# Performance work log

Hardware: AMD Instinct MI355X
Metric: run time of the kernel (lower is better)

## Reference

```python
import jax, jax.numpy as jnp
import numpy as np

N = 100000   # nodes
E = 1600000  # edges (avg degree 16)
D_IN, D_HID, D_OUT = 128, 128, 64
BN_EPS = 1e-5


def setup_inputs() -> dict:
    key = jax.random.key(0)
    ks = jax.random.split(key, 12)
    nf_mat = jax.random.normal(ks[0], (N, D_IN), dtype=jnp.float32)
    edge_index = jax.random.randint(ks[1], (2, E), 0, N, dtype=jnp.int32)
    # pre-normalized adjacency weights (GCNConv normalize=True is folded into conv_mat here)
    edge_weight = jax.random.uniform(ks[2], (E,), dtype=jnp.float32) * (1.0 / 16.0)
    def glorot(k, fan_in, fan_out):
        s = jnp.sqrt(6.0 / (fan_in + fan_out)).astype(jnp.float32)
        return jax.random.uniform(k, (fan_in, fan_out), dtype=jnp.float32, minval=-s, maxval=s)
    return {
        "nf_mat": nf_mat,
        "edge_index": edge_index,
        "edge_weight": edge_weight,
        "W0": glorot(ks[3], D_IN, D_HID), "b0": jnp.zeros((D_HID,), jnp.float32),
        "W1": glorot(ks[4], D_HID, D_HID), "b1": jnp.zeros((D_HID,), jnp.float32),
        "W2": glorot(ks[5], D_HID, D_OUT), "b2": jnp.zeros((D_OUT,), jnp.float32),
        "gamma0": jnp.ones((D_HID,), jnp.float32), "beta0": jnp.zeros((D_HID,), jnp.float32),
        "gamma1": jnp.ones((D_HID,), jnp.float32), "beta1": jnp.zeros((D_HID,), jnp.float32),
    }


def _gcn_conv(x, W, b, src, dst, w):
    # GCNConv: aggregate A_norm @ (x W) + b over the sparse edge list
    h = x @ W                                   # [N, F_out]
    msg = h[src] * w[:, None]                   # [E, F_out] gather + scale
    agg = jax.ops.segment_sum(msg, dst, num_segments=N)  # scatter-add -> [N, F_out]
    return agg + b


def _batchnorm(x, gamma, beta):
    # BatchNorm1d over node dimension (training-mode batch statistics, biased var)
    mu = jnp.mean(x, axis=0)
    var = jnp.mean(jnp.square(x - mu), axis=0)
    return gamma * (x - mu) * jax.lax.rsqrt(var + BN_EPS) + beta


def reference(nf_mat, edge_index, edge_weight, W0, b0, W1, b1, W2, b2,
              gamma0, beta0, gamma1, beta1):
    src, dst = edge_index[0], edge_index[1]
    x = nf_mat
    # layer 0: conv -> BN -> ReLU (dropout is identity in eval)
    x = _gcn_conv(x, W0, b0, src, dst, edge_weight)
    x = jax.nn.relu(_batchnorm(x, gamma0, beta0))
    # layer 1
    x = _gcn_conv(x, W1, b1, src, dst, edge_weight)
    x = jax.nn.relu(_batchnorm(x, gamma1, beta1))
    # final conv, then cross-node sum
    x = _gcn_conv(x, W2, b2, src, dst, edge_weight)
    return jnp.sum(x, axis=0)  # [D_OUT]
```

## Files before the change

### kernel.cpp

```cpp
#include <hip/hip_runtime.h>

#define BN_EPS 1e-5f

#define NPB 512
#define NPB_SHIFT 9
#define PB 512
#define WCB 200
#define WCCAP 16
#define CAP 10240
#define NSLICE 16

typedef __attribute__((ext_vector_type(8))) short short8;
typedef __attribute__((ext_vector_type(4))) float floatx4;
typedef __attribute__((ext_vector_type(2))) float floatx2;

__device__ __forceinline__ unsigned short f2bf(float f) {
    unsigned u = __float_as_uint(f);
    unsigned r = u + 0x7FFFu + ((u >> 16) & 1u);
    return (unsigned short)(r >> 16);
}
__device__ __forceinline__ float blo(unsigned v) { return __uint_as_float(v << 16); }
__device__ __forceinline__ float bhi(unsigned v) { return __uint_as_float(v & 0xffff0000u); }

__device__ __forceinline__ uint2 pk8_fp8(const float4 v0, const float4 v1) {
    int lo = 0, hi = 0;
    lo = __builtin_amdgcn_cvt_pk_fp8_f32(v0.x, v0.y, lo, false);
    lo = __builtin_amdgcn_cvt_pk_fp8_f32(v0.z, v0.w, lo, true);
    hi = __builtin_amdgcn_cvt_pk_fp8_f32(v1.x, v1.y, hi, false);
    hi = __builtin_amdgcn_cvt_pk_fp8_f32(v1.z, v1.w, hi, true);
    return make_uint2((unsigned)lo, (unsigned)hi);
}

__global__ __launch_bounds__(256) void wconv(
    const float* __restrict__ W0, const float* __restrict__ W1,
    unsigned short* __restrict__ wt0, unsigned short* __restrict__ wt1,
    float* __restrict__ stats)
{
    const int idx = blockIdx.x * 256 + threadIdx.x;
    const int n = idx >> 7, k = idx & 127;
    wt0[idx] = f2bf(W0[k * 128 + n]);
    wt1[idx] = f2bf(W1[k * 128 + n]);
    if (blockIdx.x < 11) {
        const int o = (blockIdx.x * 256 + threadIdx.x) * 4;
        *(float4*)&stats[o] = make_float4(0.f, 0.f, 0.f, 0.f);
    }
}

__global__ __launch_bounds__(256) void gemm0(
    const float* __restrict__ A, const unsigned short* __restrict__ Wt,
    uint2* __restrict__ C, int M)
{
    __shared__ char lds[53248];
    unsigned short* Al = (unsigned short*)lds;
    unsigned short* Wl = (unsigned short*)(lds + 17408);
    float* Cl = (float*)lds;

    const int tid = threadIdx.x;
    const int r0 = blockIdx.x * 64;

#pragma unroll
    for (int i = 0; i < 16; ++i) {
        const int idx = i * 256 + tid;
        const int n = idx >> 5, q = idx & 31;
        const ushort4 v = ((const ushort4*)Wt)[idx];
        *(ushort4*)&Wl[n * 136 + q * 4] = v;
    }
#pragma unroll
    for (int i = 0; i < 8; ++i) {
        const int row = i * 8 + (tid >> 5), q = tid & 31;
        const int gr = r0 + row;
        float4 v = (gr < M) ? ((const float4*)A)[(size_t)gr * 32 + q]
                            : make_float4(0.f, 0.f, 0.f, 0.f);
        ushort4 o;
        o.x = f2bf(v.x); o.y = f2bf(v.y); o.z = f2bf(v.z); o.w = f2bf(v.w);
        *(ushort4*)&Al[row * 136 + q * 4] = o;
    }
    __syncthreads();

    const int wave = tid >> 6, lane = tid & 63;
    const int lrow = lane & 15, quad = lane >> 4;
    const int n0 = wave * 32;

    floatx4 acc[4][2];
#pragma unroll
    for (int mt = 0; mt < 4; ++mt)
#pragma unroll
        for (int t = 0; t < 2; ++t)
#pragma unroll
            for (int j = 0; j < 4; ++j) acc[mt][t][j] = 0.f;

#pragma unroll
    for (int c = 0; c < 4; ++c) {
        const int k0 = c * 32;
        const short8 b0 = *(const short8*)&Wl[(n0 + lrow) * 136 + k0 + quad * 8];
        const short8 b1 = *(const short8*)&Wl[(n0 + 16 + lrow) * 136 + k0 + quad * 8];
#pragma unroll
        for (int mt = 0; mt < 4; ++mt) {
            const short8 a = *(const short8*)&Al[(mt * 16 + lrow) * 136 + k0 + quad * 8];
            acc[mt][0] = __builtin_amdgcn_mfma_f32_16x16x32_bf16(a, b0, acc[mt][0], 0, 0, 0);
            acc[mt][1] = __builtin_amdgcn_mfma_f32_16x16x32_bf16(a, b1, acc[mt][1], 0, 0, 0);
        }
    }
    __syncthreads();

#pragma unroll
    for (int mt = 0; mt < 4; ++mt)
#pragma unroll
        for (int t = 0; t < 2; ++t)
#pragma unroll
            for (int j = 0; j < 4; ++j)
                Cl[(mt * 16 + quad * 4 + j) * 132 + n0 + t * 16 + lrow] = acc[mt][t][j];
    __syncthreads();

#pragma unroll
    for (int i = 0; i < 4; ++i) {
        const int row = i * 16 + (tid >> 4);
        const int c0 = (tid & 15) * 8;
        const int gr = r0 + row;
        if (gr < M) {
            const float4 v0 = *(float4*)&Cl[row * 132 + c0];
            const float4 v1 = *(float4*)&Cl[row * 132 + c0 + 4];
            C[(size_t)gr * 16 + (c0 >> 3)] = pk8_fp8(v0, v1);
        }
    }
}

__global__ __launch_bounds__(256) void gemm1(
    const unsigned* __restrict__ Ab, const unsigned short* __restrict__ Wt,
    uint2* __restrict__ C,
    const float* __restrict__ sum, const float* __restrict__ sq,
    const float* __restrict__ g, const float* __restrict__ be,
    int M, int N)
{
    __shared__ char lds[53248];
    unsigned short* Al = (unsigned short*)lds;
    unsigned short* Wl = (unsigned short*)(lds + 17408);
    float* AscL = (float*)(lds + 52224);
    float* AshL = AscL + 128;
    float* Cl = (float*)lds;

    const int tid = threadIdx.x;
    const int r0 = blockIdx.x * 64;

    if (tid < 128) {
        float s = 0.f, q = 0.f;
#pragma unroll
        for (int k = 0; k < NSLICE; ++k) {
            s += sum[k * 128 + tid];
            q += sq[k * 128 + tid];
        }
        const float invN = 1.0f / (float)N;
        const float m = s * invN;
        const float var = q * invN - m * m;
        const float rs = rsqrtf(var + BN_EPS);
        AscL[tid] = g[tid] * rs;
        AshL[tid] = be[tid] - g[tid] * m * rs;
    }
    __syncthreads();

#pragma unroll
    for (int i = 0; i < 16; ++i) {
        const int idx = i * 256 + tid;
        const int n = idx >> 5, q = idx & 31;
        const ushort4 v = ((const ushort4*)Wt)[idx];
        *(ushort4*)&Wl[n * 136 + q * 4] = v;
    }
#pragma unroll
    for (int i = 0; i < 4; ++i) {
        const int idx = i * 256 + tid;
        const int row = idx >> 4, qc = idx & 15;
        const int gr = r0 + row;
        uint4 v = (gr < M) ? ((const uint4*)Ab)[(size_t)gr * 16 + qc]
                           : make_uint4(0, 0, 0, 0);
        const float4 a0 = *(const float4*)&AscL[qc * 8];
        const float4 a1 = *(const float4*)&AscL[qc * 8 + 4];
        const float4 b0 = *(const float4*)&AshL[qc * 8];
        const float4 b1 = *(const float4*)&AshL[qc * 8 + 4];
        float x0 = fmaxf(fmaf(a0.x, blo(v.x), b0.x), 0.f);
        float x1 = fmaxf(fmaf(a0.y, bhi(v.x), b0.y), 0.f);
        float x2 = fmaxf(fmaf(a0.z, blo(v.y), b0.z), 0.f);
        float x3 = fmaxf(fmaf(a0.w, bhi(v.y), b0.w), 0.f);
        float x4 = fmaxf(fmaf(a1.x, blo(v.z), b1.x), 0.f);
        float x5 = fmaxf(fmaf(a1.y, bhi(v.z), b1.y), 0.f);
        float x6 = fmaxf(fmaf(a1.z, blo(v.w), b1.z), 0.f);
        float x7 = fmaxf(fmaf(a1.w, bhi(v.w), b1.w), 0.f);
        uint4 o;
        o.x = (unsigned)f2bf(x0) | ((unsigned)f2bf(x1) << 16);
        o.y = (unsigned)f2bf(x2) | ((unsigned)f2bf(x3) << 16);
        o.z = (unsigned)f2bf(x4) | ((unsigned)f2bf(x5) << 16);
        o.w = (unsigned)f2bf(x6) | ((unsigned)f2bf(x7) << 16);
        *(uint4*)&Al[row * 136 + qc * 8] = o;
    }
    __syncthreads();

    const int wave = tid >> 6, lane = tid & 63;
    const int lrow = lane & 15, quad = lane >> 4;
    const int n0 = wave * 32;

    floatx4 acc[4][2];
#pragma unroll
    for (int mt = 0; mt < 4; ++mt)
#pragma unroll
        for (int t = 0; t < 2; ++t)
#pragma unroll
            for (int j = 0; j < 4; ++j) acc[mt][t][j] = 0.f;

#pragma unroll
    for (int c = 0; c < 4; ++c) {
        const int k0 = c * 32;
        const short8 b0 = *(const short8*)&Wl[(n0 + lrow) * 136 + k0 + quad * 8];
        const short8 b1 = *(const short8*)&Wl[(n0 + 16 + lrow) * 136 + k0 + quad * 8];
#pragma unroll
        for (int mt = 0; mt < 4; ++mt) {
            const short8 a = *(const short8*)&Al[(mt * 16 + lrow) * 136 + k0 + quad * 8];
            acc[mt][0] = __builtin_amdgcn_mfma_f32_16x16x32_bf16(a, b0, acc[mt][0], 0, 0, 0);
            acc[mt][1] = __builtin_amdgcn_mfma_f32_16x16x32_bf16(a, b1, acc[mt][1], 0, 0, 0);
        }
    }
    __syncthreads();

#pragma unroll
    for (int mt = 0; mt < 4; ++mt)
#pragma unroll
        for (int t = 0; t < 2; ++t)
#pragma unroll
            for (int j = 0; j < 4; ++j)
                Cl[(mt * 16 + quad * 4 + j) * 132 + n0 + t * 16 + lrow] = acc[mt][t][j];
    __syncthreads();

#pragma unroll
    for (int i = 0; i < 4; ++i) {
        const int row = i * 16 + (tid >> 4);
        const int c0 = (tid & 15) * 8;
        const int gr = r0 + row;
        if (gr < M) {
            const float4 v0 = *(float4*)&Cl[row * 132 + c0];
            const float4 v1 = *(float4*)&Cl[row * 132 + c0 + 4];
            C[(size_t)gr * 16 + (c0 >> 3)] = pk8_fp8(v0, v1);
        }
    }
}

__global__ __launch_bounds__(512) void bucket_build(
    const int* __restrict__ src, const int* __restrict__ dst,
    const float* __restrict__ ew,
    int* __restrict__ gDg, int* __restrict__ gSg,
    uint2* __restrict__ bktD, uint2* __restrict__ bktS, int E, int B, int chunk)
{
    __shared__ uint2 buf[WCB][WCCAP + 1];
    __shared__ int tail[WCB], gcur[WCB];
    const int tid = threadIdx.x;
    const bool isD = (int)blockIdx.x < PB;
    const int blk = isD ? blockIdx.x : (blockIdx.x - PB);
    const int* __restrict__ key = isD ? dst : src;
    int* __restrict__ gG = isD ? gDg : gSg;
    uint2* __restrict__ bkt = isD ? bktD : bktS;

    for (int i = tid; i < B; i += 512) tail[i] = 0;
    __syncthreads();
    const int lo = blk * chunk;
    const int hi = min(E, lo + chunk);
    for (int e = lo + tid; e < hi; e += 512)
        atomicAdd(&tail[key[e] >> NPB_SHIFT], 1);
    __syncthreads();
    for (int i = tid; i < B; i += 512)
        gcur[i] = i * CAP + atomicAdd(&gG[i], tail[i]);
    __syncthreads();
    for (int i = tid; i < B; i += 512) tail[i] = 0;
    __syncthreads();
    const int nt = (hi - lo + 1023) >> 10;
    for (int t = 0; t < nt; ++t) {
#pragma unroll
        for (int jj = 0; jj < 2; ++jj) {
            const int e = lo + t * 1024 + jj * 512 + tid;
            if (e < hi) {
                const int s = src[e];
                const unsigned wb = __float_as_uint(ew[e]);
                int b; uint2 r;
                if (isD) {
                    const int d = dst[e];
                    b = d >> NPB_SHIFT;
                    r = make_uint2(((unsigned)s << NPB_SHIFT) | (unsigned)(d & (NPB - 1)), wb);
                } else {
                    b = s >> NPB_SHIFT;
                    r = make_uint2((unsigned)(s & (NPB - 1)), wb);
                }
                const int p = atomicAdd(&tail[b], 1);
                if (p < WCCAP) buf[b][p] = r;
                else           bkt[gcur[b] + p] = r;
            }
        }
        __syncthreads();
        const bool last = (t == nt - 1);
        for (int x = tid; x < B * WCCAP; x += 512) {
            const int bb = x >> 4, i = x & (WCCAP - 1);
            const int nb = min(tail[bb], WCCAP);
            const int k = last ? nb : (nb & ~7);
            if (i < k) bkt[gcur[bb] + i] = buf[bb][i];
        }
        __syncthreads();
        if (tid < B) {
            const int tl = tail[tid];
            const int nb = min(tl, WCCAP);
            const int k = last ? nb : (nb & ~7);
            const int adv = (tl > WCCAP) ? tl : k;
            const int left = (tl > WCCAP) ? 0 : (tl - k);
            for (int i = 0; i < left; ++i) buf[tid][i] = buf[tid][k + i];
            gcur[tid] += adv; tail[tid] = left;
        }
        __syncthreads();
    }
}

__global__ __launch_bounds__(256) void bucket_scan(
    const int* __restrict__ gDg, const int* __restrict__ gSg,
    int* __restrict__ baseD, int* __restrict__ baseS, int B, int E)
{
    __shared__ int lD[256], lS[256];
    const int tid = threadIdx.x;
    const int sD = (tid < B) ? gDg[tid] : 0;
    const int sS = (tid < B) ? gSg[tid] : 0;
    lD[tid] = sD; lS[tid] = sS;
    __syncthreads();
    for (int st = 1; st < 256; st <<= 1) {
        const int vD = (tid >= st) ? lD[tid - st] : 0;
        const int vS = (tid >= st) ? lS[tid - st] : 0;
        __syncthreads();
        lD[tid] += vD; lS[tid] += vS;
        __syncthreads();
    }
    if (tid < B) { baseD[tid] = lD[tid] - sD; baseS[tid] = lS[tid] - sS; }
    if (tid == 0) { baseD[B] = E; baseS[B] = E; }
}

__global__ __launch_bounds__(512) void bucket_sortcw(
    const uint2* __restrict__ bktD, const int* __restrict__ baseD,
    const int* __restrict__ gDg,
    int* __restrict__ rp, int2* __restrict__ packed,
    const uint2* __restrict__ bktS, const int* __restrict__ gSg,
    float* __restrict__ cw, int N, int B)
{
    const int tid = threadIdx.x;
    if (blockIdx.x >= B) {
        const int b = blockIdx.x - B;
        const int lo = b * CAP;
        const int cntS = gSg[b];
        __shared__ float sm[NPB];
        sm[tid] = 0.f;
        __syncthreads();
        for (int i = tid; i < cntS; i += 512) {
            const uint2 r = bktS[lo + i];
            atomicAdd(&sm[r.x], __uint_as_float(r.y));
        }
        __syncthreads();
        const int n0 = b * NPB + tid;
        if (n0 < N) cw[n0] = sm[tid];
        return;
    }
    const int b = blockIdx.x;
    const int lor = b * CAP;
    const int sz = gDg[b];
    const int wb = baseD[b];
    __shared__ int cnt[NPB], cur[NPB];
    __shared__ int2 stage[CAP];
    cnt[tid] = 0;
    __syncthreads();
    for (int i = tid; i < sz; i += 512)
        atomicAdd(&cnt[bktD[lor + i].x & (NPB - 1)], 1);
    __syncthreads();
    int* ls = (int*)stage;
    const int c = cnt[tid];
    ls[tid] = c;
    __syncthreads();
    for (int st = 1; st < NPB; st <<= 1) {
        const int v = (tid >= st) ? ls[tid - st] : 0;
        __syncthreads();
        ls[tid] += v;
        __syncthreads();
    }
    const int incl = ls[tid];
    __syncthreads();
    {
        const int n0 = b * NPB + tid;
        if (n0 < N) rp[n0] = wb + incl;
        cur[tid] = incl - c;
    }
    __syncthreads();
    if (sz <= CAP) {
        for (int i = tid; i < sz; i += 512) {
            const uint2 r = bktD[lor + i];
            const int pos = atomicAdd(&cur[r.x & (NPB - 1)], 1);
            stage[pos] = make_int2((int)(r.x >> NPB_SHIFT) << 4, (int)r.y);
        }
        __syncthreads();
        for (int i = tid; i < sz; i += 512)
            packed[wb + i] = stage[i];
    } else {
        for (int i = tid; i < sz; i += 512) {
            const uint2 r = bktD[lor + i];
            const int pos = atomicAdd(&cur[r.x & (NPB - 1)], 1);
            packed[wb + pos] = make_int2((int)(r.x >> NPB_SHIFT) << 4, (int)r.y);
        }
    }
}


#define ACC_EDGE(V, W, A) do { \
    floatx2 w2_; w2_.x = (W); w2_.y = (W); \
    floatx2 f_; \
    f_ = __builtin_amdgcn_cvt_pk_f32_fp8((int)(V).x, false); \
    A[0] = f_ * w2_ + A[0]; \
    f_ = __builtin_amdgcn_cvt_pk_f32_fp8((int)(V).x, true);  \
    A[1] = f_ * w2_ + A[1]; \
    f_ = __builtin_amdgcn_cvt_pk_f32_fp8((int)(V).y, false); \
    A[2] = f_ * w2_ + A[2]; \
    f_ = __builtin_amdgcn_cvt_pk_f32_fp8((int)(V).y, true);  \
    A[3] = f_ * w2_ + A[3]; \
} while (0)

__global__ __launch_bounds__(256) void aggq(
    const int2* __restrict__ packed, const int* __restrict__ rp,
    const uint2* __restrict__ h2, uint4* __restrict__ aggb4,
    float* __restrict__ sum, float* __restrict__ sq, int N)
{
    __shared__ int2 eb[16][65];
    __shared__ float lsum[512], lsq[512];

    const int tid = threadIdx.x;
    const int lane = tid & 63, wave = tid >> 6;
    const int sub = lane >> 4;
    const int u = lane & 15;
    const int wq = wave * 4 + sub;
    const int nb0 = blockIdx.x * 32;
    const int nX = nb0 + wq * 2, nY = nX + 1;
    int2* ebq = eb[wq];

    int rpv = 0;
    {
        const int idx = nb0 - 1 + lane;
        if (lane <= 32 && idx >= 0 && idx < N) rpv = rp[idx];
    }
    const int sX = __shfl(rpv, 2 * wq, 64);
    const int eX = __shfl(rpv, 2 * wq + 1, 64);
    const int eYr = __shfl(rpv, 2 * wq + 2, 64);
    const int sY = eX;
    const int dXf = max(eX - sX, 0), dYf = max(eYr - sY, 0);
    const int eXe = sX + dXf, eYe = sY + dYf;

    {
        int2 r;
        r = (u      < dXf) ? packed[sX + u]      : make_int2(0, 0); ebq[u]      = r;
        r = (u + 16 < dXf) ? packed[sX + 16 + u] : make_int2(0, 0); ebq[16 + u] = r;
        r = (u      < dYf) ? packed[sY + u]      : make_int2(0, 0); ebq[32 + u] = r;
        r = (u + 16 < dYf) ? packed[sY + 16 + u] : make_int2(0, 0); ebq[48 + u] = r;
    }

    floatx2 aX[4], aY[4];
#pragma unroll
    for (int k = 0; k < 4; ++k) { aX[k] = 0.f; aY[k] = 0.f; }

    const int cX = min(dXf, 32), cY = min(dYf, 32);
    const int jmax = (cX > cY) ? cX : cY;

    for (int j = 0; j < jmax; j += 4) {
        const int2 x0 = ebq[j],      x1 = ebq[j + 1];
        const int2 x2 = ebq[j + 2],  x3 = ebq[j + 3];
        const int2 y0 = ebq[32 + j],     y1 = ebq[32 + j + 1];
        const int2 y2 = ebq[32 + j + 2], y3 = ebq[32 + j + 3];
        const uint2 vx0 = h2[(size_t)(unsigned)(x0.x + u)];
        const uint2 vx1 = h2[(size_t)(unsigned)(x1.x + u)];
        const uint2 vx2 = h2[(size_t)(unsigned)(x2.x + u)];
        const uint2 vx3 = h2[(size_t)(unsigned)(x3.x + u)];
        const uint2 vy0 = h2[(size_t)(unsigned)(y0.x + u)];
        const uint2 vy1 = h2[(size_t)(unsigned)(y1.x + u)];
        const uint2 vy2 = h2[(size_t)(unsigned)(y2.x + u)];
        const uint2 vy3 = h2[(size_t)(unsigned)(y3.x + u)];
        ACC_EDGE(vx0, __int_as_float(x0.y), aX);
        ACC_EDGE(vx1, __int_as_float(x1.y), aX);
        ACC_EDGE(vx2, __int_as_float(x2.y), aX);
        ACC_EDGE(vx3, __int_as_float(x3.y), aX);
        ACC_EDGE(vy0, __int_as_float(y0.y), aY);
        ACC_EDGE(vy1, __int_as_float(y1.y), aY);
        ACC_EDGE(vy2, __int_as_float(y2.y), aY);
        ACC_EDGE(vy3, __int_as_float(y3.y), aY);
    }

    for (int base = sX + 32; base < eXe; base += 32) {
        const int rem = eXe - base;
        int2 r;
        r = (u      < rem) ? packed[base + u]      : make_int2(0, 0); ebq[u]      = r;
        r = (u + 16 < rem) ? packed[base + 16 + u] : make_int2(0, 0); ebq[16 + u] = r;
        const int cc = min(rem, 32);
        for (int j = 0; j < cc; j += 4) {
            const int2 x0 = ebq[j], x1 = ebq[j + 1], x2 = ebq[j + 2], x3 = ebq[j + 3];
            const uint2 v0 = h2[(size_t)(unsigned)(x0.x + u)];
            const uint2 v1 = h2[(size_t)(unsigned)(x1.x + u)];
            const uint2 v2 = h2[(size_t)(unsigned)(x2.x + u)];
            const uint2 v3 = h2[(size_t)(unsigned)(x3.x + u)];
            ACC_EDGE(v0, __int_as_float(x0.y), aX);
            ACC_EDGE(v1, __int_as_float(x1.y), aX);
            ACC_EDGE(v2, __int_as_float(x2.y), aX);
            ACC_EDGE(v3, __int_as_float(x3.y), aX);
        }
    }
    for (int base = sY + 32; base < eYe; base += 32) {
        const int rem = eYe - base;
        int2 r;
        r = (u      < rem) ? packed[base + u]      : make_int2(0, 0); ebq[32 + u] = r;
        r = (u + 16 < rem) ? packed[base + 16 + u] : make_int2(0, 0); ebq[48 + u] = r;
        const int cc = min(rem, 32);
        for (int j = 0; j < cc; j += 4) {
            const int2 y0 = ebq[32 + j], y1 = ebq[32 + j + 1];
            const int2 y2 = ebq[32 + j + 2], y3 = ebq[32 + j + 3];
            const uint2 v0 = h2[(size_t)(unsigned)(y0.x + u)];
            const uint2 v1 = h2[(size_t)(unsigned)(y1.x + u)];
            const uint2 v2 = h2[(size_t)(unsigned)(y2.x + u)];
            const uint2 v3 = h2[(size_t)(unsigned)(y3.x + u)];
            ACC_EDGE(v0, __int_as_float(y0.y), aY);
            ACC_EDGE(v1, __int_as_float(y1.y), aY);
            ACC_EDGE(v2, __int_as_float(y2.y), aY);
            ACC_EDGE(v3, __int_as_float(y3.y), aY);
        }
    }

    if (nX < N) {
        uint4 o;
        o.x = (unsigned)f2bf(aX[0].x) | ((unsigned)f2bf(aX[0].y) << 16);
        o.y = (unsigned)f2bf(aX[1].x) | ((unsigned)f2bf(aX[1].y) << 16);
        o.z = (unsigned)f2bf(aX[2].x) | ((unsigned)f2bf(aX[2].y) << 16);
        o.w = (unsigned)f2bf(aX[3].x) | ((unsigned)f2bf(aX[3].y) << 16);
        aggb4[(size_t)nX * 16 + u] = o;
    }
    if (nY < N) {
        uint4 o;
        o.x = (unsigned)f2bf(aY[0].x) | ((unsigned)f2bf(aY[0].y) << 16);
        o.y = (unsigned)f2bf(aY[1].x) | ((unsigned)f2bf(aY[1].y) << 16);
        o.z = (unsigned)f2bf(aY[2].x) | ((unsigned)f2bf(aY[2].y) << 16);
        o.w = (unsigned)f2bf(aY[3].x) | ((unsigned)f2bf(aY[3].y) << 16);
        aggb4[(size_t)nY * 16 + u] = o;
    }

    floatx2 cs0 = aX[0] + aY[0], cs1 = aX[1] + aY[1];
    floatx2 cs2 = aX[2] + aY[2], cs3 = aX[3] + aY[3];
    floatx2 cq0 = aX[0] * aX[0] + aY[0] * aY[0];
    floatx2 cq1 = aX[1] * aX[1] + aY[1] * aY[1];
    floatx2 cq2 = aX[2] * aX[2] + aY[2] * aY[2];
    floatx2 cq3 = aX[3] * aX[3] + aY[3] * aY[3];
#define XRED(V) \
    V.x += __shfl_xor(V.x, 16, 64); V.y += __shfl_xor(V.y, 16, 64); \
    V.x += __shfl_xor(V.x, 32, 64); V.y += __shfl_xor(V.y, 32, 64);
    XRED(cs0) XRED(cs1) XRED(cs2) XRED(cs3)
    XRED(cq0) XRED(cq1) XRED(cq2) XRED(cq3)
#undef XRED
    const floatx2 ws = (sub == 0) ? cs0 : (sub == 1) ? cs1 : (sub == 2) ? cs2 : cs3;
    const floatx2 wwq = (sub == 0) ? cq0 : (sub == 1) ? cq1 : (sub == 2) ? cq2 : cq3;
    const int col = u * 8 + 2 * sub;
    lsum[wave * 128 + col] = ws.x;  lsum[wave * 128 + col + 1] = ws.y;
    lsq[wave * 128 + col]  = wwq.x; lsq[wave * 128 + col + 1]  = wwq.y;
    __syncthreads();
    if (tid < 128) {
        float s = 0.f, q = 0.f;
#pragma unroll
        for (int i = 0; i < 4; ++i) {
            s += lsum[i * 128 + tid];
            q += lsq[i * 128 + tid];
        }
        const int sl = (blockIdx.x & (NSLICE - 1)) * 128;
        atomicAdd(&sum[sl + tid], s);
        atomicAdd(&sq[sl + tid], q);
    }
}

__global__ __launch_bounds__(256) void wcolsum_bf16(
    const uint2* __restrict__ xb2, const float* __restrict__ cw,
    const float* __restrict__ sum1, const float* __restrict__ sq1,
    const float* __restrict__ g, const float* __restrict__ be,
    float* __restrict__ sout, int N)
{
    __shared__ float Aaf[128], Baf[128];
    __shared__ float4 ls[256];
    const int tid = threadIdx.x;
    if (tid < 128) {
        float s = 0.f, q = 0.f;
#pragma unroll
        for (int k = 0; k < NSLICE; ++k) {
            s += sum1[k * 128 + tid];
            q += sq1[k * 128 + tid];
        }
        const float invN = 1.0f / (float)N;
        const float m = s * invN;
        const float var = q * invN - m * m;
        const float rs = rsqrtf(var + BN_EPS);
        Aaf[tid] = g[tid] * rs;
        Baf[tid] = be[tid] - g[tid] * m * rs;
    }
    __syncthreads();
    const int u2 = tid & 31;
    const int half = (tid >> 5) & 1;
    const int rr = tid >> 6;
    const float4 A = *(const float4*)&Aaf[u2 * 4];
    const float4 Bv = *(const float4*)&Baf[u2 * 4];
    float4 s = make_float4(0.f, 0.f, 0.f, 0.f);
    for (int row = blockIdx.x * 8 + rr * 2 + half; row < N; row += gridDim.x * 8) {
        const uint2 v = xb2[(size_t)row * 32 + u2];
        const float c = cw[row];
        s.x = fmaf(c, fmaxf(fmaf(A.x, blo(v.x), Bv.x), 0.f), s.x);
        s.y = fmaf(c, fmaxf(fmaf(A.y, bhi(v.x), Bv.y), 0.f), s.y);
        s.z = fmaf(c, fmaxf(fmaf(A.z, blo(v.y), Bv.z), 0.f), s.z);
        s.w = fmaf(c, fmaxf(fmaf(A.w, bhi(v.y), Bv.w), 0.f), s.w);
    }
    ls[tid] = s;
    __syncthreads();
    if (tid < 32) {
        float4 a = ls[tid];
#pragma unroll
        for (int k = 1; k < 8; ++k) {
            const float4 b = ls[tid + 32 * k];
            a.x += b.x; a.y += b.y; a.z += b.z; a.w += b.w;
        }
        float* so = sout + (blockIdx.x & (NSLICE - 1)) * 128 + tid * 4;
        atomicAdd(&so[0], a.x);
        atomicAdd(&so[1], a.y);
        atomicAdd(&so[2], a.z);
        atomicAdd(&so[3], a.w);
    }
}

__global__ void final_out(
    const float* __restrict__ s, const float* __restrict__ W2,
    const float* __restrict__ b2, float* __restrict__ out, int N, int Dout)
{
    __shared__ float sv[128];
    const int j = threadIdx.x;
    {
        float a = 0.f;
#pragma unroll
        for (int k = 0; k < NSLICE; ++k) a += s[k * 128 + j];
        sv[j] = a;
    }
    __syncthreads();
    if (j < Dout) {
        float acc = 0.f;
        for (int f = 0; f < 128; ++f) acc = fmaf(sv[f], W2[f * Dout + j], acc);
        out[j] = acc + (float)N * b2[j];
    }
}

extern "C" void kernel_launch(void* const* d_in, const int* in_sizes, int n_in,
                              void* d_out, int out_size, void* d_ws, size_t ws_size,
                              hipStream_t stream)
{
    const float* nf  = (const float*)d_in[0];
    const int*   ei  = (const int*)d_in[1];
    const float* ew  = (const float*)d_in[2];
    const float* W0  = (const float*)d_in[3];
    const float* W1  = (const float*)d_in[5];
    const float* W2  = (const float*)d_in[7];
    const float* b2  = (const float*)d_in[8];
    const float* g0  = (const float*)d_in[9];
    const float* be0 = (const float*)d_in[10];
    const float* g1  = (const float*)d_in[11];
    const float* be1 = (const float*)d_in[12];

    const int N = in_sizes[0] / 128;
    const int E = in_sizes[2];
    const int* srcI = ei;
    const int* dstI = ei + E;

    const int B = (N + NPB - 1) / NPB;
    const int chunk = (E + PB - 1) / PB;

    const size_t HB = ((size_t)N * 128 * 2 + 255) & ~(size_t)255;
    const size_t NA = ((size_t)N * sizeof(int) + 255) & ~(size_t)255;
    const size_t BKB = ((size_t)B * CAP * 8 + 255) & ~(size_t)255;
    char* ws = (char*)d_ws;
    size_t off = 0;
    float* cw    = (float*)(ws + off); off += NA;
    int*   rp    = (int*)  (ws + off); off += NA;
    float* stats = (float*)(ws + off); off += 45056;
    int*   baseD = (int*)  (ws + off); off += 2048;
    int*   baseS = (int*)  (ws + off); off += 2048;
    uint2* hbuf  = (uint2*)(ws + off); off += HB;
    unsigned* aggb = (unsigned*)(ws + off); off += HB;
    int2*  packed = (int2*)(ws + off); off += (size_t)E * 8;
    uint2* bktD  = (uint2*)(ws + off); off += BKB;
    uint2* bktS  = (uint2*)(ws + off); off += BKB;
    unsigned short* wt0 = (unsigned short*)(ws + off); off += 32768;
    unsigned short* wt1 = (unsigned short*)(ws + off); off += 32768;
    (void)ws_size;

    float* sum0 = stats + 0 * NSLICE * 128;
    float* sq0  = stats + 1 * NSLICE * 128;
    float* sum1 = stats + 2 * NSLICE * 128;
    float* sq1  = stats + 3 * NSLICE * 128;
    float* svec = stats + 4 * NSLICE * 128;
    int*   gDg  = (int*)(stats + 5 * NSLICE * 128);
    int*   gSg  = (int*)(stats + 5 * NSLICE * 128) + 256;

    const int gemmGrid = (N + 63) / 64;
    const int aggGrid  = (N + 31) / 32;

    wconv<<<64, 256, 0, stream>>>(W0, W1, wt0, wt1, stats);

    bucket_build<<<2 * PB, 512, 0, stream>>>(srcI, dstI, ew, gDg, gSg,
                                             bktD, bktS, E, B, chunk);
    bucket_scan<<<1, 256, 0, stream>>>(gDg, gSg, baseD, baseS, B, E);
    bucket_sortcw<<<2 * B, 512, 0, stream>>>(bktD, baseD, gDg, rp, packed,
                                             bktS, gSg, cw, N, B);

    gemm0<<<gemmGrid, 256, 0, stream>>>(nf, wt0, hbuf, N);
    aggq<<<aggGrid, 256, 0, stream>>>(
        packed, rp, (const uint2*)hbuf, (uint4*)aggb, sum0, sq0, N);

    gemm1<<<gemmGrid, 256, 0, stream>>>(aggb, wt1, hbuf, sum0, sq0, g0, be0, N, N);
    aggq<<<aggGrid, 256, 0, stream>>>(
        packed, rp, (const uint2*)hbuf, (uint4*)aggb, sum1, sq1, N);

    wcolsum_bf16<<<2048, 256, 0, stream>>>((const uint2*)aggb, cw, sum1, sq1,
                                           g1, be1, svec, N);
    final_out<<<1, 128, 0, stream>>>(svec, W2, b2, (float*)d_out, N, out_size);
}
```

Baseline: 299.4 us.

## Fold bucket scan into sort kernel and hold bucket records in registers

Drops the separate single-block bucket_scan launch. Each sort block now loads all bucket counts into shared memory and computes its own prefix offset with a serial loop. In the common path (bucket fits CAP) each thread loads its edge records once into a register array and reuses them for both the counting and scatter passes, avoiding a second global read. The cost is extra register pressure from RPT=20 int2 values per thread, plus a redundant serial sum in every block.

```diff
diff --git a/kernel.cpp b/kernel.cpp
--- a/kernel.cpp
+++ b/kernel.cpp
@@ -8,6 +8,7 @@
 #define WCB 200
 #define WCCAP 16
 #define CAP 10240
+#define RPT 20
 #define NSLICE 16
 
 typedef __attribute__((ext_vector_type(8))) short short8;
@@ -312,30 +313,8 @@
     }
 }
 
-__global__ __launch_bounds__(256) void bucket_scan(
-    const int* __restrict__ gDg, const int* __restrict__ gSg,
-    int* __restrict__ baseD, int* __restrict__ baseS, int B, int E)
-{
-    __shared__ int lD[256], lS[256];
-    const int tid = threadIdx.x;
-    const int sD = (tid < B) ? gDg[tid] : 0;
-    const int sS = (tid < B) ? gSg[tid] : 0;
-    lD[tid] = sD; lS[tid] = sS;
-    __syncthreads();
-    for (int st = 1; st < 256; st <<= 1) {
-        const int vD = (tid >= st) ? lD[tid - st] : 0;
-        const int vS = (tid >= st) ? lS[tid - st] : 0;
-        __syncthreads();
-        lD[tid] += vD; lS[tid] += vS;
-        __syncthreads();
-    }
-    if (tid < B) { baseD[tid] = lD[tid] - sD; baseS[tid] = lS[tid] - sS; }
-    if (tid == 0) { baseD[B] = E; baseS[B] = E; }
-}
-
 __global__ __launch_bounds__(512) void bucket_sortcw(
-    const uint2* __restrict__ bktD, const int* __restrict__ baseD,
-    const int* __restrict__ gDg,
+    const uint2* __restrict__ bktD, const int* __restrict__ gDg,
     int* __restrict__ rp, int2* __restrict__ packed,
     const uint2* __restrict__ bktS, const int* __restrict__ gSg,
     float* __restrict__ cw, int N, int B)
@@ -359,43 +338,78 @@
     }
     const int b = blockIdx.x;
     const int lor = b * CAP;
-    const int sz = gDg[b];
-    const int wb = baseD[b];
     __shared__ int cnt[NPB], cur[NPB];
     __shared__ int2 stage[CAP];
+    cur[tid] = (tid < B) ? gDg[tid] : 0;
     cnt[tid] = 0;
     __syncthreads();
-    for (int i = tid; i < sz; i += 512)
-        atomicAdd(&cnt[bktD[lor + i].x & (NPB - 1)], 1);
-    __syncthreads();
-    int* ls = (int*)stage;
-    const int c = cnt[tid];
-    ls[tid] = c;
-    __syncthreads();
-    for (int st = 1; st < NPB; st <<= 1) {
-        const int v = (tid >= st) ? ls[tid - st] : 0;
-        __syncthreads();
-        ls[tid] += v;
-        __syncthreads();
-    }
-    const int incl = ls[tid];
-    __syncthreads();
-    {
-        const int n0 = b * NPB + tid;
-        if (n0 < N) rp[n0] = wb + incl;
-        cur[tid] = incl - c;
-    }
-    __syncthreads();
+    const int sz = cur[b];
+    int wb = 0;
+    for (int i = 0; i < b; ++i) wb += cur[i];
+    __syncthreads();
+
     if (sz <= CAP) {
-        for (int i = tid; i < sz; i += 512) {
-            const uint2 r = bktD[lor + i];
-            const int pos = atomicAdd(&cur[r.x & (NPB - 1)], 1);
-            stage[pos] = make_int2((int)(r.x >> NPB_SHIFT) << 4, (int)r.y);
+        int2 rec[RPT];
+#pragma unroll
+        for (int k = 0; k < RPT; ++k) {
+            const int i = k * 512 + tid;
+            rec[k] = (i < sz) ? *(const int2*)&bktD[lor + i] : make_int2(0, 0);
+        }
+#pragma unroll
+        for (int k = 0; k < RPT; ++k)
+            if (k * 512 + tid < sz) atomicAdd(&cnt[rec[k].x & (NPB - 1)], 1);
+        __syncthreads();
+        int* ls = (int*)stage;
+        const int c = cnt[tid];
+        ls[tid] = c;
+        __syncthreads();
+        for (int st = 1; st < NPB; st <<= 1) {
+            const int v = (tid >= st) ? ls[tid - st] : 0;
+            __syncthreads();
+            ls[tid] += v;
+            __syncthreads();
+        }
+        const int incl = ls[tid];
+        __syncthreads();
+        {
+            const int n0 = b * NPB + tid;
+            if (n0 < N) rp[n0] = wb + incl;
+            cur[tid] = incl - c;
+        }
+        __syncthreads();
+#pragma unroll
+        for (int k = 0; k < RPT; ++k) {
+            if (k * 512 + tid < sz) {
+                const int2 r = rec[k];
+                const int pos = atomicAdd(&cur[r.x & (NPB - 1)], 1);
+                stage[pos] = make_int2((int)((unsigned)r.x >> NPB_SHIFT) << 4, r.y);
+            }
         }
         __syncthreads();
         for (int i = tid; i < sz; i += 512)
             packed[wb + i] = stage[i];
     } else {
+        for (int i = tid; i < sz; i += 512)
+            atomicAdd(&cnt[bktD[lor + i].x & (NPB - 1)], 1);
+        __syncthreads();
+        int* ls = (int*)stage;
+        const int c = cnt[tid];
+        ls[tid] = c;
+        __syncthreads();
+        for (int st = 1; st < NPB; st <<= 1) {
+            const int v = (tid >= st) ? ls[tid - st] : 0;
+            __syncthreads();
+            ls[tid] += v;
+            __syncthreads();
+        }
+        const int incl = ls[tid];
+        __syncthreads();
+        {
+            const int n0 = b * NPB + tid;
+            if (n0 < N) rp[n0] = wb + incl;
+            cur[tid] = incl - c;
+        }
+        __syncthreads();
         for (int i = tid; i < sz; i += 512) {
             const uint2 r = bktD[lor + i];
             const int pos = atomicAdd(&cur[r.x & (NPB - 1)], 1);
@@ -678,8 +692,6 @@
     float* cw    = (float*)(ws + off); off += NA;
     int*   rp    = (int*)  (ws + off); off += NA;
     float* stats = (float*)(ws + off); off += 45056;
-    int*   baseD = (int*)  (ws + off); off += 2048;
-    int*   baseS = (int*)  (ws + off); off += 2048;
     uint2* hbuf  = (uint2*)(ws + off); off += HB;
     unsigned* aggb = (unsigned*)(ws + off); off += HB;
     int2*  packed = (int2*)(ws + off); off += (size_t)E * 8;
@@ -704,8 +716,7 @@
 
     bucket_build<<<2 * PB, 512, 0, stream>>>(srcI, dstI, ew, gDg, gSg,
                                              bktD, bktS, E, B, chunk);
-    bucket_scan<<<1, 256, 0, stream>>>(gDg, gSg, baseD, baseS, B, E);
-    bucket_sortcw<<<2 * B, 512, 0, stream>>>(bktD, baseD, gDg, rp, packed,
+    bucket_sortcw<<<2 * B, 512, 0, stream>>>(bktD, gDg, rp, packed,
                                              bktS, gSg, cw, N, B);
 
     gemm0<<<gemmGrid, 256, 0, stream>>>(nf, wt0, hbuf, N);
```

New measurement: 292.3 us. -2.4%, faster.
